# Performance work log

Measured on AMD Instinct MI355X. Metric: run time of the kernel, lower is better.

## Reference

```python
import jax, jax.numpy as jnp
import numpy as np

PATCH = 8
C1 = 1e-4
C2 = 1e-3
EPS = 1e-3
ALPHA = 0.4
WEIGHTS = (1.0, 0.01, 1.0)


def charbonnier(x):
    return (x * x + EPS * EPS) ** ALPHA


def resize_bilinear_ac(img, H2, W2):
    # bilinear resize with align_corners=True (matches F.interpolate)
    B, C, H, W = img.shape
    fy = jnp.arange(H2, dtype=img.dtype) * ((H - 1) / max(H2 - 1, 1))
    fx = jnp.arange(W2, dtype=img.dtype) * ((W - 1) / max(W2 - 1, 1))
    y0 = jnp.clip(jnp.floor(fy).astype(jnp.int32), 0, H - 2)
    x0 = jnp.clip(jnp.floor(fx).astype(jnp.int32), 0, W - 2)
    wy = (fy - y0)[None, None, :, None]
    wx = (fx - x0)[None, None, None, :]
    rows = img[:, :, y0, :] * (1 - wy) + img[:, :, y0 + 1, :] * wy  # [B,C,H2,W]
    out = rows[:, :, :, x0] * (1 - wx) + rows[:, :, :, x0 + 1] * wx  # [B,C,H2,W2]
    return out


def bilinear_warp(img, flow):
    # backward warp: sample img at (x + u, y + v), bilinear, border clamp
    B, C, H, W = img.shape
    gx = jnp.arange(W, dtype=img.dtype)[None, None, :] + flow[:, 0]  # [B,H,W]
    gy = jnp.arange(H, dtype=img.dtype)[None, :, None] + flow[:, 1]  # [B,H,W]
    x0f = jnp.floor(gx)
    y0f = jnp.floor(gy)
    wx = (gx - x0f)[:, None]  # [B,1,H,W]
    wy = (gy - y0f)[:, None]
    x0 = jnp.clip(x0f.astype(jnp.int32), 0, W - 1)
    x1 = jnp.clip(x0 + 1, 0, W - 1)
    y0 = jnp.clip(y0f.astype(jnp.int32), 0, H - 1)
    y1 = jnp.clip(y0 + 1, 0, H - 1)
    imgf = img.reshape(B, C, H * W)

    def gather(yi, xi):
        idx = (yi * W + xi).reshape(B, 1, H * W)
        g = jnp.take_along_axis(imgf, jnp.broadcast_to(idx, (B, C, H * W)), axis=2)
        return g.reshape(B, C, H, W)

    v00 = gather(y0, x0)
    v01 = gather(y0, x1)
    v10 = gather(y1, x0)
    v11 = gather(y1, x1)
    top = v00 * (1 - wx) + v01 * wx
    bot = v10 * (1 - wx) + v11 * wx
    return top * (1 - wy) + bot * wy


def torch_gradient(x, axis):
    # torch.gradient: central diff interior, one-sided at edges, spacing 1
    n = x.shape[axis]
    sl = lambda a, b: jax.lax.slice_in_dim(x, a, b, axis=axis)
    first = sl(1, 2) - sl(0, 1)
    interior = (sl(2, n) - sl(0, n - 2)) * 0.5
    last = sl(n - 1, n) - sl(n - 2, n - 1)
    return jnp.concatenate([first, interior, last], axis=axis)


def ssim_score(I1, I2):
    # faithful to SSIMLoss: stats pooled over ALL non-overlapping patches per
    # (batch, channel), i.e. over the region cropped to multiples of patch.
    B, C, H, W = I1.shape
    p = min(PATCH, H)
    PH, PW = H // p, W // p
    x = I1[:, :, :PH * p, :PW * p].reshape(B, C, -1)
    y = I2[:, :, :PH * p, :PW * p].reshape(B, C, -1)
    N = x.shape[-1]
    mu1 = x.mean(-1)
    mu2 = y.mean(-1)
    d1 = x - mu1[..., None]
    d2 = y - mu2[..., None]
    var1 = (d1 * d1).sum(-1) / (N - 1)  # torch .var() is unbiased
    var2 = (d2 * d2).sum(-1) / (N - 1)
    s12 = (d1 * d2).mean(-1)
    num = (2 * mu1 * mu2 + C1) * (2 * s12 + C2)
    den = (mu1 ** 2 + mu2 ** 2 + C1) * (var1 + var2 + C2)
    return num / den  # [B, C]


def setup_inputs() -> dict:
    key = jax.random.key(0)
    k1, k2 = jax.random.split(key)
    images = jax.random.uniform(k1, (16, 33, 256, 256), dtype=jnp.float32)
    flows = jax.random.normal(k2, (16, 20, 128, 128), dtype=jnp.float32)
    return {"images": images, "flows": flows}


def reference(images, flows):
    B, Cf, FH, FW = flows.shape
    n_flows = Cf // 2  # 10 frame pairs
    imgs = resize_bilinear_ac(images, FH, FW)  # [B,33,FH,FW]
    src = imgs[:, 3:].reshape(B * n_flows, 3, FH, FW)
    fl = flows.reshape(B * n_flows, 2, FH, FW)
    warped = bilinear_warp(src, fl).reshape(B, n_flows * 3, FH, FW)
    ref = imgs[:, : n_flows * 3]

    similarity_loss = ssim_score(ref, warped).mean()

    flow_x = flows[:, 0::2]
    flow_y = flows[:, 1::2]
    smooth = (charbonnier(torch_gradient(flow_x, 1))
              + charbonnier(torch_gradient(flow_x, 2))
              + charbonnier(torch_gradient(flow_y, 1))
              + charbonnier(torch_gradient(flow_y, 2))).mean()

    pixel_loss = charbonnier(ref - warped).mean()

    return WEIGHTS[0] * pixel_loss + WEIGHTS[1] * smooth + WEIGHTS[2] * similarity_loss
```

## Files before the change

### kernel.cpp

```cpp
#include <hip/hip_runtime.h>

#define IH 256
#define IW 256
#define FH 128
#define FW 128
#define NB 16
#define ICH 33
#define NF 10
#define NC 30
#define PL (FH * FW)
#define LOSS_BLOCKS (NB * NC * 2)
#define SMOOTH_BLOCKS 240
#define HALO 7
#define SROWS (64 + 2 * HALO + 1)
#define PART_STRIDE 8

__device__ __forceinline__ float charb(float g) {
    float t = fmaf(g, g, 1e-6f);
    return __builtin_amdgcn_exp2f(0.4f * __builtin_amdgcn_logf(t));
}

__device__ __forceinline__ float resized_at(const float* __restrict__ plane, int Y, int X) {
    const float s = (float)(255.0 / 127.0);
    float fy = (float)Y * s;
    float fx = (float)X * s;
    int y0 = (int)fy; y0 = y0 > IH - 2 ? IH - 2 : y0;
    int x0 = (int)fx; x0 = x0 > IW - 2 ? IW - 2 : x0;
    float wy = fy - (float)y0;
    float wx = fx - (float)x0;
    const float* p0 = plane + y0 * IW + x0;
    float v00 = p0[0], v01 = p0[1];
    float v10 = p0[IW], v11 = p0[IW + 1];
    float r0 = v00 * (1.f - wy) + v10 * wy;
    float r1 = v01 * (1.f - wy) + v11 * wy;
    return r0 * (1.f - wx) + r1 * wx;
}

__global__ void __launch_bounds__(256) mega(const float* __restrict__ images,
                                            const float* __restrict__ flows,
                                            float* __restrict__ ws)
{
    float* part_loss   = ws;
    float* part_smooth = ws + LOSS_BLOCKS * PART_STRIDE;

    if (blockIdx.x >= LOSS_BLOCKS) {
        int sb = blockIdx.x - LOSS_BLOCKS;
        const int total = NB * NF * PL;
        float s = 0.f;
        for (int i = sb * 256 + threadIdx.x; i < total; i += SMOOTH_BLOCKS * 256) {
            int w = i & (FW - 1);
            int h = (i >> 7) & (FH - 1);
            int f = (i >> 14) % NF;
            int b = i / (NF * PL);
            int pix = h * FW + w;
            const float* xp = flows + (size_t)(b * 2 * NF + 2 * f) * PL;
            const float* yp = xp + PL;

            float g1x, g1y;
            if (f == 0)           { g1x = xp[2 * PL + pix] - xp[pix];
                                    g1y = yp[2 * PL + pix] - yp[pix]; }
            else if (f == NF - 1) { g1x = xp[pix] - xp[pix - 2 * PL];
                                    g1y = yp[pix] - yp[pix - 2 * PL]; }
            else                  { g1x = 0.5f * (xp[2 * PL + pix] - xp[pix - 2 * PL]);
                                    g1y = 0.5f * (yp[2 * PL + pix] - yp[pix - 2 * PL]); }

            float g2x, g2y;
            if (h == 0)           { g2x = xp[pix + FW] - xp[pix];
                                    g2y = yp[pix + FW] - yp[pix]; }
            else if (h == FH - 1) { g2x = xp[pix] - xp[pix - FW];
                                    g2y = yp[pix] - yp[pix - FW]; }
            else                  { g2x = 0.5f * (xp[pix + FW] - xp[pix - FW]);
                                    g2y = 0.5f * (yp[pix + FW] - yp[pix - FW]); }

            s += charb(g1x) + charb(g2x) + charb(g1y) + charb(g2y);
        }
        for (int off = 32; off > 0; off >>= 1) s += __shfl_down(s, off, 64);
        __shared__ float shs[4];
        int wave = threadIdx.x >> 6;
        if ((threadIdx.x & 63) == 0) shs[wave] = s;
        __syncthreads();
        if (threadIdx.x == 0)
            part_smooth[sb] = shs[0] + shs[1] + shs[2] + shs[3];
        return;
    }

    __shared__ float slds[SROWS * FW];
    int blk = blockIdx.x;
    int bc = blk >> 1;
    int p  = blk & 1;
    int b = bc / NC;
    int c = bc % NC;
    int f = c / 3;
    const float* ref_img  = images + (size_t)(b * ICH + c) * (IH * IW);
    const float* src_img  = images + (size_t)(b * ICH + 3 + c) * (IH * IW);
    const float* fx_plane = flows + (size_t)(b * 2 * NF + 2 * f) * PL;
    const float* fy_plane = fx_plane + PL;

    int lo = p * 64 - HALO;          if (lo < 0) lo = 0;
    int hi = p * 64 + 63 + HALO + 1; if (hi > FH - 1) hi = FH - 1;
    int nstage = (hi - lo + 1) * FW;

    for (int i = threadIdx.x; i < nstage; i += 256) {
        int y = lo + (i >> 7);
        int x = i & (FW - 1);
        slds[i] = resized_at(src_img, y, x);
    }
    __syncthreads();

    float s_ref = 0.f, s_w = 0.f, s_r2 = 0.f, s_w2 = 0.f, s_rw = 0.f, s_pix = 0.f;
    int base = p * 8192;
    for (int i = threadIdx.x; i < 8192; i += 256) {
        int px = base + i;
        int h = px >> 7;
        int w = px & (FW - 1);
        float ref = resized_at(ref_img, h, w);
        float gx = (float)w + fx_plane[px];
        float gy = (float)h + fy_plane[px];
        float x0f = floorf(gx), y0f = floorf(gy);
        float wx = gx - x0f, wy = gy - y0f;
        int x0 = (int)x0f; x0 = min(max(x0, 0), FW - 1);
        int y0 = (int)y0f; y0 = min(max(y0, 0), FH - 1);
        int x1 = min(x0 + 1, FW - 1);
        int y1 = min(y0 + 1, FH - 1);
        float v00, v01, v10, v11;
        if (y0 >= lo && y1 <= hi) {
            const float* r0 = slds + ((y0 - lo) << 7);
            const float* r1 = slds + ((y1 - lo) << 7);
            v00 = r0[x0]; v01 = r0[x1];
            v10 = r1[x0]; v11 = r1[x1];
        } else {
            v00 = resized_at(src_img, y0, x0);
            v01 = resized_at(src_img, y0, x1);
            v10 = resized_at(src_img, y1, x0);
            v11 = resized_at(src_img, y1, x1);
        }
        float top = v00 * (1.f - wx) + v01 * wx;
        float bot = v10 * (1.f - wx) + v11 * wx;
        float wv = top * (1.f - wy) + bot * wy;

        s_ref += ref; s_w += wv;
        s_r2 += ref * ref; s_w2 += wv * wv; s_rw += ref * wv;
        s_pix += charb(ref - wv);
    }
    for (int off = 32; off > 0; off >>= 1) {
        s_ref += __shfl_down(s_ref, off, 64);
        s_w   += __shfl_down(s_w, off, 64);
        s_r2  += __shfl_down(s_r2, off, 64);
        s_w2  += __shfl_down(s_w2, off, 64);
        s_rw  += __shfl_down(s_rw, off, 64);
        s_pix += __shfl_down(s_pix, off, 64);
    }
    __shared__ float sh[4][6];
    int wave = threadIdx.x >> 6;
    if ((threadIdx.x & 63) == 0) {
        sh[wave][0] = s_ref; sh[wave][1] = s_w; sh[wave][2] = s_r2;
        sh[wave][3] = s_w2;  sh[wave][4] = s_rw; sh[wave][5] = s_pix;
    }
    __syncthreads();
    if (threadIdx.x < 6) {
        int k = threadIdx.x;
        part_loss[blk * PART_STRIDE + k] =
            sh[0][k] + sh[1][k] + sh[2][k] + sh[3][k];
    }
}

__global__ void __launch_bounds__(512) finalize2(const float* __restrict__ ws,
                                                 float* __restrict__ out)
{
    const float* part_loss   = ws;
    const float* part_smooth = ws + LOSS_BLOCKS * PART_STRIDE;
    int tid = threadIdx.x;
    float ssim = 0.f, pix = 0.f, smo = 0.f;
    if (tid < NB * NC) {
        const float* a0 = part_loss + (2 * tid) * PART_STRIDE;
        const float* a1 = a0 + PART_STRIDE;
        float t0 = a0[0] + a1[0];
        float t1 = a0[1] + a1[1];
        float t2 = a0[2] + a1[2];
        float t3 = a0[3] + a1[3];
        float t4 = a0[4] + a1[4];
        pix = a0[5] + a1[5];
        const float N = (float)PL;
        float mu1 = t0 / N, mu2 = t1 / N;
        float var1 = (t2 - t0 * mu1) / (N - 1.f);
        float var2 = (t3 - t1 * mu2) / (N - 1.f);
        float s12 = t4 / N - mu1 * mu2;
        float num = (2.f * mu1 * mu2 + 1e-4f) * (2.f * s12 + 1e-3f);
        float den = (mu1 * mu1 + mu2 * mu2 + 1e-4f) * (var1 + var2 + 1e-3f);
        ssim = num / den;
    }
    if (tid < SMOOTH_BLOCKS) smo = part_smooth[tid];
    __shared__ float sa[512], sb[512], sc[512];
    sa[tid] = ssim; sb[tid] = pix; sc[tid] = smo;
    __syncthreads();
    for (int off = 256; off > 0; off >>= 1) {
        if (tid < off) {
            sa[tid] += sa[tid + off];
            sb[tid] += sb[tid + off];
            sc[tid] += sc[tid + off];
        }
        __syncthreads();
    }
    if (tid == 0) {
        out[0] = sb[0] / (float)(NB * NC * PL)
               + 0.01f * (sc[0] / (float)(NB * NF * PL))
               + sa[0] / (float)(NB * NC);
    }
}

extern "C" void kernel_launch(void* const* d_in, const int* in_sizes, int n_in,
                              void* d_out, int out_size, void* d_ws, size_t ws_size,
                              hipStream_t stream) {
    const float* images = (const float*)d_in[0];
    const float* flows  = (const float*)d_in[1];
    float* ws = (float*)d_ws;
    mega<<<LOSS_BLOCKS + SMOOTH_BLOCKS, 256, 0, stream>>>(images, flows, ws);
    finalize2<<<1, 512, 0, stream>>>(ws, (float*)d_out);
}
```

Measured before the change: 253.5 us.

## Split warp-loss work into quarter planes, process two pixels per thread, reorder blocks

Each (batch, channel) plane is now split across four blocks instead of two, so LDS staging covers 32 rows plus halo and there are twice as many loss blocks. Each thread handles two adjacent pixels per iteration. It hoists the x-interpolation weights of the reference resize, loads flows as float2, and shares the row computation across both pixels. Smooth blocks are moved to the front of the grid and launch bounds request occupancy 6. The aim is better load balance and occupancy and fewer redundant address computations, at the cost of more halo restaging overhead per plane.

```diff
diff --git a/kernel.cpp b/kernel.cpp
--- a/kernel.cpp
+++ b/kernel.cpp
@@ -9,10 +9,11 @@
 #define NF 10
 #define NC 30
 #define PL (FH * FW)
-#define LOSS_BLOCKS (NB * NC * 2)
+#define SPLIT 4
+#define LOSS_BLOCKS (NB * NC * SPLIT)
 #define SMOOTH_BLOCKS 240
 #define HALO 7
-#define SROWS (64 + 2 * HALO + 1)
+#define SROWS (32 + 2 * HALO + 1)
 #define PART_STRIDE 8
 
 __device__ __forceinline__ float charb(float g) {
@@ -36,15 +37,15 @@
     return r0 * (1.f - wx) + r1 * wx;
 }
 
-__global__ void __launch_bounds__(256) mega(const float* __restrict__ images,
-                                            const float* __restrict__ flows,
-                                            float* __restrict__ ws)
+__global__ void __launch_bounds__(256, 6) mega(const float* __restrict__ images,
+                                               const float* __restrict__ flows,
+                                               float* __restrict__ ws)
 {
     float* part_loss   = ws;
     float* part_smooth = ws + LOSS_BLOCKS * PART_STRIDE;
 
-    if (blockIdx.x >= LOSS_BLOCKS) {
-        int sb = blockIdx.x - LOSS_BLOCKS;
+    if (blockIdx.x < SMOOTH_BLOCKS) {
+        int sb = blockIdx.x;
         const int total = NB * NF * PL;
         float s = 0.f;
         for (int i = sb * 256 + threadIdx.x; i < total; i += SMOOTH_BLOCKS * 256) {
@@ -85,9 +86,9 @@
     }
 
     __shared__ float slds[SROWS * FW];
-    int blk = blockIdx.x;
-    int bc = blk >> 1;
-    int p  = blk & 1;
+    int blk = blockIdx.x - SMOOTH_BLOCKS;
+    int bc = blk >> 2;
+    int p  = blk & 3;
     int b = bc / NC;
     int c = bc % NC;
     int f = c / 3;
@@ -96,10 +97,11 @@
     const float* fx_plane = flows + (size_t)(b * 2 * NF + 2 * f) * PL;
     const float* fy_plane = fx_plane + PL;
 
-    int lo = p * 64 - HALO;          if (lo < 0) lo = 0;
-    int hi = p * 64 + 63 + HALO + 1; if (hi > FH - 1) hi = FH - 1;
+    int lo = p * 32 - HALO;          if (lo < 0) lo = 0;
+    int hi = p * 32 + 31 + HALO + 1; if (hi > FH - 1) hi = FH - 1;
     int nstage = (hi - lo + 1) * FW;
 
+    #pragma unroll 2
     for (int i = threadIdx.x; i < nstage; i += 256) {
         int y = lo + (i >> 7);
         int x = i & (FW - 1);
@@ -107,40 +109,72 @@
     }
     __syncthreads();
 
+    const float sR = (float)(255.0 / 127.0);
+    int w0 = (2 * threadIdx.x) & (FW - 1);
+    float fx0 = (float)w0 * sR;
+    float fx1 = (float)(w0 + 1) * sR;
+    int x00 = (int)fx0; if (x00 > IW - 2) x00 = IW - 2;
+    int x01 = (int)fx1; if (x01 > IW - 2) x01 = IW - 2;
+    float wxr0 = fx0 - (float)x00;
+    float wxr1 = fx1 - (float)x01;
+
     float s_ref = 0.f, s_w = 0.f, s_r2 = 0.f, s_w2 = 0.f, s_rw = 0.f, s_pix = 0.f;
-    int base = p * 8192;
-    for (int i = threadIdx.x; i < 8192; i += 256) {
-        int px = base + i;
+    int base2 = p * 2048;
+    for (int i = threadIdx.x; i < 2048; i += 256) {
+        int p2 = base2 + i;
+        int px = 2 * p2;
         int h = px >> 7;
-        int w = px & (FW - 1);
-        float ref = resized_at(ref_img, h, w);
-        float gx = (float)w + fx_plane[px];
-        float gy = (float)h + fy_plane[px];
-        float x0f = floorf(gx), y0f = floorf(gy);
-        float wx = gx - x0f, wy = gy - y0f;
-        int x0 = (int)x0f; x0 = min(max(x0, 0), FW - 1);
-        int y0 = (int)y0f; y0 = min(max(y0, 0), FH - 1);
-        int x1 = min(x0 + 1, FW - 1);
-        int y1 = min(y0 + 1, FH - 1);
-        float v00, v01, v10, v11;
-        if (y0 >= lo && y1 <= hi) {
-            const float* r0 = slds + ((y0 - lo) << 7);
-            const float* r1 = slds + ((y1 - lo) << 7);
-            v00 = r0[x0]; v01 = r0[x1];
-            v10 = r1[x0]; v11 = r1[x1];
-        } else {
-            v00 = resized_at(src_img, y0, x0);
-            v01 = resized_at(src_img, y0, x1);
-            v10 = resized_at(src_img, y1, x0);
-            v11 = resized_at(src_img, y1, x1);
-        }
-        float top = v00 * (1.f - wx) + v01 * wx;
-        float bot = v10 * (1.f - wx) + v11 * wx;
-        float wv = top * (1.f - wy) + bot * wy;
-
-        s_ref += ref; s_w += wv;
-        s_r2 += ref * ref; s_w2 += wv * wv; s_rw += ref * wv;
-        s_pix += charb(ref - wv);
+        float fyR = (float)h * sR;
+        int yr0 = (int)fyR; if (yr0 > IH - 2) yr0 = IH - 2;
+        float wyr = fyR - (float)yr0;
+        const float* rp0 = ref_img + yr0 * IW;
+        const float* rp1 = rp0 + IW;
+        float a00 = rp0[x00], a01 = rp0[x00 + 1], a10 = rp1[x00], a11 = rp1[x00 + 1];
+        float b00 = rp0[x01], b01 = rp0[x01 + 1], b10 = rp1[x01], b11 = rp1[x01 + 1];
+        float2 fl_x = ((const float2*)fx_plane)[p2];
+        float2 fl_y = ((const float2*)fy_plane)[p2];
+
+        float ar0 = a00 * (1.f - wyr) + a10 * wyr;
+        float ar1 = a01 * (1.f - wyr) + a11 * wyr;
+        float ref0 = ar0 * (1.f - wxr0) + ar1 * wxr0;
+        float br0 = b00 * (1.f - wyr) + b10 * wyr;
+        float br1 = b01 * (1.f - wyr) + b11 * wyr;
+        float ref1 = br0 * (1.f - wxr1) + br1 * wxr1;
+
+        float wv[2];
+        #pragma unroll
+        for (int q = 0; q < 2; q++) {
+            float gx = (float)(w0 + q) + (q ? fl_x.y : fl_x.x);
+            float gy = (float)h + (q ? fl_y.y : fl_y.x);
+            float x0f = floorf(gx), y0f = floorf(gy);
+            float wx = gx - x0f, wy = gy - y0f;
+            int x0 = (int)x0f; x0 = min(max(x0, 0), FW - 1);
+            int y0 = (int)y0f; y0 = min(max(y0, 0), FH - 1);
+            int x1 = min(x0 + 1, FW - 1);
+            int y1 = min(y0 + 1, FH - 1);
+            float v00, v01, v10, v11;
+            if (y0 >= lo && y1 <= hi) {
+                const float* r0 = slds + ((y0 - lo) << 7);
+                const float* r1 = slds + ((y1 - lo) << 7);
+                v00 = r0[x0]; v01 = r0[x1];
+                v10 = r1[x0]; v11 = r1[x1];
+            } else {
+                v00 = resized_at(src_img, y0, x0);
+                v01 = resized_at(src_img, y0, x1);
+                v10 = resized_at(src_img, y1, x0);
+                v11 = resized_at(src_img, y1, x1);
+            }
+            float top = v00 * (1.f - wx) + v01 * wx;
+            float bot = v10 * (1.f - wx) + v11 * wx;
+            wv[q] = top * (1.f - wy) + bot * wy;
+        }
+
+        s_ref += ref0 + ref1;
+        s_w   += wv[0] + wv[1];
+        s_r2  += ref0 * ref0 + ref1 * ref1;
+        s_w2  += wv[0] * wv[0] + wv[1] * wv[1];
+        s_rw  += ref0 * wv[0] + ref1 * wv[1];
+        s_pix += charb(ref0 - wv[0]) + charb(ref1 - wv[1]);
     }
     for (int off = 32; off > 0; off >>= 1) {
         s_ref += __shfl_down(s_ref, off, 64);
@@ -159,8 +193,7 @@
     __syncthreads();
     if (threadIdx.x < 6) {
         int k = threadIdx.x;
-        part_loss[blk * PART_STRIDE + k] =
-            sh[0][k] + sh[1][k] + sh[2][k] + sh[3][k];
+        part_loss[blk * PART_STRIDE + k] = sh[0][k] + sh[1][k] + sh[2][k] + sh[3][k];
     }
 }
 
@@ -172,14 +205,12 @@
     int tid = threadIdx.x;
     float ssim = 0.f, pix = 0.f, smo = 0.f;
     if (tid < NB * NC) {
-        const float* a0 = part_loss + (2 * tid) * PART_STRIDE;
-        const float* a1 = a0 + PART_STRIDE;
-        float t0 = a0[0] + a1[0];
-        float t1 = a0[1] + a1[1];
-        float t2 = a0[2] + a1[2];
-        float t3 = a0[3] + a1[3];
-        float t4 = a0[4] + a1[4];
-        pix = a0[5] + a1[5];
+        float t0 = 0, t1 = 0, t2 = 0, t3 = 0, t4 = 0;
+        for (int q = 0; q < SPLIT; q++) {
+            const float* a = part_loss + (SPLIT * tid + q) * PART_STRIDE;
+            t0 += a[0]; t1 += a[1]; t2 += a[2]; t3 += a[3]; t4 += a[4];
+            pix += a[5];
+        }
         const float N = (float)PL;
         float mu1 = t0 / N, mu2 = t1 / N;
         float var1 = (t2 - t0 * mu1) / (N - 1.f);
@@ -214,6 +245,6 @@
     const float* images = (const float*)d_in[0];
     const float* flows  = (const float*)d_in[1];
     float* ws = (float*)d_ws;
-    mega<<<LOSS_BLOCKS + SMOOTH_BLOCKS, 256, 0, stream>>>(images, flows, ws);
+    mega<<<SMOOTH_BLOCKS + LOSS_BLOCKS, 256, 0, stream>>>(images, flows, ws);
     finalize2<<<1, 512, 0, stream>>>(ws, (float*)d_out);
 }
```

Result: faster. 233.0 us (-8.1%).
